# Performance work log

Hardware: AMD Instinct MI355X
Metric: run time of the kernel (lower is better)

## Reference

```python
import jax, jax.numpy as jnp
import numpy as np

E = float(np.e)  # torch.exp(torch.tensor(1.0))

def setup_inputs() -> dict:
    key = jax.random.key(0)
    k1, k2 = jax.random.split(key)
    b, t, d = 4, 4096, 256
    x = jax.random.normal(k1, (b, t, d), dtype=jnp.float32)
    padding_mask = jnp.zeros((b, 1, t), dtype=jnp.float32)  # additive mask: 0 valid, -inf-like for pad
    W_in = jax.random.normal(k2, (d, d), dtype=jnp.float32) * (1.0 / np.sqrt(d))
    b_in = jnp.zeros((d,), dtype=jnp.float32)
    return {"x": x, "padding_mask": padding_mask, "W_in": W_in, "b_in": b_in}

def reference(x, padding_mask, W_in, b_in):
    b, t, d = x.shape
    x = x @ W_in.T + b_in  # proj_in
    n = jnp.arange(1, t + 1, dtype=x.dtype)  # linspace(1,t,t)
    dist = jnp.abs(n[None, :] - n[:, None])  # [t,t] |i-j|
    tg = -dist[None, :, :] + padding_mask    # [b,t,t] via broadcast
    attn = jnp.exp(tg / E)                   # exponential distance decay, no softmax
    return jnp.matmul(attn, x)               # [b,t,d]
```

## Files before the change

kernel.cpp:

```cpp
#include <hip/hip_runtime.h>

#define TT 4096
#define DD 256
#define BT 64
#define HW 64
#define WIN (BT + 2*HW)
#define YP (DD + 8)
#define WP 40

typedef __attribute__((ext_vector_type(8))) short short8;
typedef __attribute__((ext_vector_type(4))) float f32x4;

__device__ __forceinline__ unsigned short f2bf(float f) {
    unsigned int u = __builtin_bit_cast(unsigned int, f);
    u += 0x7fffu + ((u >> 16) & 1u);
    return (unsigned short)(u >> 16);
}
__device__ __forceinline__ float bf2f(unsigned short h) {
    unsigned int u = ((unsigned int)h) << 16;
    return __builtin_bit_cast(float, u);
}

__global__ __launch_bounds__(512, 2)
void distattn_kernel(const float* __restrict__ x,
                     const float* __restrict__ mask,
                     const float* __restrict__ Win,
                     const float* __restrict__ bin,
                     float* __restrict__ out)
{
    __shared__ float yF[BT][DD + 1];
    __shared__ unsigned short yB[BT][YP];
    __shared__ unsigned short Wl[2][DD][WP];
    __shared__ float wv[WIN];
    __shared__ float rp[WIN];
    __shared__ float sp[8][BT];
    __shared__ float s_l[BT];

    const int tid  = threadIdx.x;
    const int b    = blockIdx.x >> 6;
    const int r0   = (blockIdx.x & 63) * BT;
    const int base = r0 - HW;

    const float INV_E = 0.36787944117144233f;
    const float R     = 0.69220062755534635f;

    if (tid < WIN) {
        rp[tid] = __expf(-(float)tid * INV_E);
        int j = base + tid;
        wv[tid] = (j >= 0 && j < TT) ? __expf(mask[b * TT + j] * INV_E) : 0.0f;
    }
    __syncthreads();

    if (tid < 256) {
        const int c = tid;
        const float* xb = x + (size_t)b * TT * DD + c;
        float f = 0.0f;
        #pragma unroll 8
        for (int t = 0; t < HW; ++t) {
            int jc = max(base + t, 0);
            f = fmaf(R, f, xb[(size_t)jc * DD] * wv[t]);
        }
        #pragma unroll 8
        for (int t = HW; t < HW + BT; ++t) {
            int j = base + t;
            f = fmaf(R, f, xb[(size_t)j * DD] * wv[t]);
            yF[t - HW][c] = f;
        }
    } else {
        const int c = tid - 256;
        const float* xb = x + (size_t)b * TT * DD + c;
        float bb = 0.0f;
        #pragma unroll 8
        for (int t = WIN - 1; t >= HW + BT; --t) {
            int jc = min(base + t, TT - 1);
            bb = fmaf(R, bb, xb[(size_t)jc * DD] * wv[t]);
        }
        #pragma unroll 8
        for (int t = HW + BT - 1; t >= HW; --t) {
            int j = base + t;
            float v = xb[(size_t)j * DD] * wv[t];
            bb = fmaf(R, bb, v);
            yB[t - HW][c] = f2bf(bb - v);
        }
    }

    {
        int row = tid & 63, q = tid >> 6;
        float s = 0.0f;
        #pragma unroll 8
        for (int tt = 0; tt < 24; ++tt) {
            int t = 24 * q + tt;
            int d = row + HW - t; d = (d < 0) ? -d : d;
            s = fmaf(rp[d], wv[t], s);
        }
        sp[q][row] = s;
    }

    auto stage = [&](int c, int bufsel) {
        #pragma unroll
        for (int it = 0; it < 4; ++it) {
            int e   = tid + (it << 9);
            int row = e >> 3;
            int kp  = e & 7;
            float4 w4 = *reinterpret_cast<const float4*>(&Win[row * DD + 32 * c + 4 * kp]);
            uint2 p;
            p.x = (unsigned)f2bf(w4.x) | ((unsigned)f2bf(w4.y) << 16);
            p.y = (unsigned)f2bf(w4.z) | ((unsigned)f2bf(w4.w) << 16);
            *reinterpret_cast<uint2*>(&Wl[bufsel][row][4 * kp]) = p;
        }
    };

    stage(0, 0);
    __syncthreads();

    #pragma unroll
    for (int e = 0; e < 32; ++e) {
        int idx = (e << 9) | tid;
        int i = idx >> 8, c = idx & 255;
        yB[i][c] = f2bf(yF[i][c] + bf2f(yB[i][c]));
    }
    if (tid < BT) {
        float s = 0.0f;
        #pragma unroll
        for (int q = 0; q < 8; ++q) s += sp[q][tid];
        s_l[tid] = s;
    }
    __syncthreads();

    const int w  = tid >> 6;
    const int lane = tid & 63;
    const int lr = lane & 15;
    const int lg = lane >> 4;
    const int wr = w >> 2;
    const int wc = w & 3;

    f32x4 acc[2][4];
    #pragma unroll
    for (int m = 0; m < 2; ++m)
        #pragma unroll
        for (int n = 0; n < 4; ++n) acc[m][n] = (f32x4){0.f, 0.f, 0.f, 0.f};

    for (int kk = 0; kk < 8; ++kk) {
        if (kk < 7) stage(kk + 1, (kk + 1) & 1);
        short8 afr[2], bfr[4];
        #pragma unroll
        for (int m = 0; m < 2; ++m)
            afr[m] = *reinterpret_cast<const short8*>(&yB[32 * wr + 16 * m + lr][kk * 32 + lg * 8]);
        #pragma unroll
        for (int n = 0; n < 4; ++n)
            bfr[n] = *reinterpret_cast<const short8*>(&Wl[kk & 1][64 * wc + 16 * n + lr][lg * 8]);
        #pragma unroll
        for (int m = 0; m < 2; ++m)
            #pragma unroll
            for (int n = 0; n < 4; ++n)
                acc[m][n] = __builtin_amdgcn_mfma_f32_16x16x32_bf16(afr[m], bfr[n], acc[m][n], 0, 0, 0);
        __syncthreads();
    }

    float bcol[4];
    #pragma unroll
    for (int n = 0; n < 4; ++n) bcol[n] = bin[64 * wc + 16 * n + lr];
    float* ob = out + ((size_t)b * TT + r0) * DD;
    #pragma unroll
    for (int m = 0; m < 2; ++m) {
        #pragma unroll
        for (int j = 0; j < 4; ++j) {
            int i = 32 * wr + 16 * m + lg * 4 + j;
            float si = s_l[i];
            #pragma unroll
            for (int n = 0; n < 4; ++n)
                ob[(size_t)i * DD + 64 * wc + 16 * n + lr] = acc[m][n][j] + si * bcol[n];
        }
    }
}

extern "C" void kernel_launch(void* const* d_in, const int* in_sizes, int n_in,
                              void* d_out, int out_size, void* d_ws, size_t ws_size,
                              hipStream_t stream) {
    const float* x    = (const float*)d_in[0];
    const float* mask = (const float*)d_in[1];
    const float* Win  = (const float*)d_in[2];
    const float* bin  = (const float*)d_in[3];
    float* out = (float*)d_out;

    const int nb = in_sizes[0] / (TT * DD);
    hipLaunchKernelGGL(distattn_kernel, dim3(nb * (TT / BT)), dim3(512), 0, stream,
                       x, mask, Win, bin, out);
}
```

Measured before the change: 25.25 us.

## Replace serial decay recurrences with banded MFMA matmul using split-bf16 inputs

The forward and backward exponential-decay scans over the 192-row window are replaced by a banded matrix product on MFMA. Decay weights come from a bf16 lookup table, and x is split into hi and lo bf16 parts to keep precision. The loads of x and W are double-buffered in registers and LDS with swizzled layouts, and blockIdx is remapped. This removes the long serial dependency chains, at the cost of extra MFMA work and bf16 rounding of the decay coefficients.

```diff
diff --git a/kernel.cpp b/kernel.cpp
--- a/kernel.cpp
+++ b/kernel.cpp
@@ -4,21 +4,23 @@
 #define DD 256
 #define BT 64
 #define HW 64
-#define WIN (BT + 2*HW)
-#define YP (DD + 8)
-#define WP 40
+#define WIN 192
 
 typedef __attribute__((ext_vector_type(8))) short short8;
 typedef __attribute__((ext_vector_type(4))) float f32x4;
-
-__device__ __forceinline__ unsigned short f2bf(float f) {
+typedef __attribute__((ext_vector_type(4))) unsigned int u32x4;
+
+__device__ __forceinline__ unsigned int f2bf(float f) {
     unsigned int u = __builtin_bit_cast(unsigned int, f);
     u += 0x7fffu + ((u >> 16) & 1u);
-    return (unsigned short)(u >> 16);
-}
-__device__ __forceinline__ float bf2f(unsigned short h) {
-    unsigned int u = ((unsigned int)h) << 16;
+    return u >> 16;
+}
+__device__ __forceinline__ float bf2f(unsigned int h) {
+    unsigned int u = h << 16;
     return __builtin_bit_cast(float, u);
+}
+__device__ __forceinline__ int qswz(int row, int q) {
+    return row * 64 + ((q ^ ((row >> 1) & 3)) << 4);
 }
 
 __global__ __launch_bounds__(512, 2)
@@ -28,66 +30,104 @@
                      const float* __restrict__ bin,
                      float* __restrict__ out)
 {
-    __shared__ float yF[BT][DD + 1];
-    __shared__ unsigned short yB[BT][YP];
-    __shared__ unsigned short Wl[2][DD][WP];
+    __shared__ __align__(16) unsigned short xT[2][256][32];
+    __shared__ __align__(16) unsigned short yB[64][256];
+    __shared__ __align__(16) unsigned short Wl[2][256][32];
     __shared__ float wv[WIN];
     __shared__ float rp[WIN];
+    __shared__ unsigned short rpb[WIN];
     __shared__ float sp[8][BT];
     __shared__ float s_l[BT];
 
     const int tid  = threadIdx.x;
-    const int b    = blockIdx.x >> 6;
-    const int r0   = (blockIdx.x & 63) * BT;
+    const int orig = blockIdx.x;
+    const int wg   = (orig & 7) * 32 + (orig >> 3);
+    const int b    = wg >> 6;
+    const int r0   = (wg & 63) * BT;
     const int base = r0 - HW;
 
+    const int w  = tid >> 6, lane = tid & 63;
+    const int lr = lane & 15, lg = lane >> 4;
+    const int wr = w >> 2,   wc = w & 3;
+
     const float INV_E = 0.36787944117144233f;
-    const float R     = 0.69220062755534635f;
 
     if (tid < WIN) {
-        rp[tid] = __expf(-(float)tid * INV_E);
+        float rv = __expf(-(float)tid * INV_E);
+        rp[tid]  = rv;
+        rpb[tid] = (unsigned short)f2bf(rv);
         int j = base + tid;
         wv[tid] = (j >= 0 && j < TT) ? __expf(mask[b * TT + j] * INV_E) : 0.0f;
     }
+
+    const int c    = tid >> 1;
+    const int half = tid & 1;
+    const float* xcol = x + (size_t)b * TT * DD + c;
+
+    auto xload = [&](int ch, float* xv) {
+        int t0 = ch * 16 + half * 8;
+        #pragma unroll
+        for (int s = 0; s < 8; ++s) {
+            int j = base + t0 + s;
+            j = min(max(j, 0), TT - 1);
+            xv[s] = xcol[(size_t)j * DD];
+        }
+    };
+    auto xstore = [&](int ch, const float* xv, int buf) {
+        int t0 = ch * 16 + half * 8;
+        unsigned int pk[8];
+        #pragma unroll
+        for (int s = 0; s < 8; ++s) {
+            float v = xv[s] * wv[t0 + s];
+            unsigned int hi = f2bf(v);
+            float lo = v - bf2f(hi);
+            pk[s] = (hi & 0xffffu) | (f2bf(lo) << 16);
+        }
+        char* bp = (char*)(&xT[buf][0][0]);
+        *(u32x4*)(bp + qswz(c, 2 * half))     = (u32x4){pk[0], pk[1], pk[2], pk[3]};
+        *(u32x4*)(bp + qswz(c, 2 * half + 1)) = (u32x4){pk[4], pk[5], pk[6], pk[7]};
+    };
+
+    f32x4 acc1[2][4];
+    #pragma unroll
+    for (int m = 0; m < 2; ++m)
+        #pragma unroll
+        for (int n = 0; n < 4; ++n) acc1[m][n] = (f32x4){0.f, 0.f, 0.f, 0.f};
+
+    auto p1mm = [&](int ch, int buf) {
+        short8 afr[2], bfr[4];
+        #pragma unroll
+        for (int m = 0; m < 2; ++m) {
+            int i = 32 * wr + 16 * m + lr;
+            unsigned short a[4];
+            #pragma unroll
+            for (int jj = 0; jj < 4; ++jj) {
+                int d = i + HW - (ch * 16 + 4 * lg + jj);
+                d = d < 0 ? -d : d;
+                a[jj] = rpb[d];
+            }
+            afr[m] = (short8){(short)a[0], (short)a[0], (short)a[1], (short)a[1],
+                              (short)a[2], (short)a[2], (short)a[3], (short)a[3]};
+        }
+        const char* bp = (const char*)(&xT[buf][0][0]);
+        #pragma unroll
+        for (int n = 0; n < 4; ++n)
+            bfr[n] = *(const short8*)(bp + qswz(64 * wc + 16 * n + lr, lg));
+        #pragma unroll
+        for (int m = 0; m < 2; ++m)
+            #pragma unroll
+            for (int n = 0; n < 4; ++n)
+                acc1[m][n] = __builtin_amdgcn_mfma_f32_16x16x32_bf16(afr[m], bfr[n], acc1[m][n], 0, 0, 0);
+    };
+
+    float rA[8], rB[8];
+    xload(0, rA);
     __syncthreads();
-
-    if (tid < 256) {
-        const int c = tid;
-        const float* xb = x + (size_t)b * TT * DD + c;
-        float f = 0.0f;
-        #pragma unroll 8
-        for (int t = 0; t < HW; ++t) {
-            int jc = max(base + t, 0);
-            f = fmaf(R, f, xb[(size_t)jc * DD] * wv[t]);
-        }
-        #pragma unroll 8
-        for (int t = HW; t < HW + BT; ++t) {
-            int j = base + t;
-            f = fmaf(R, f, xb[(size_t)j * DD] * wv[t]);
-            yF[t - HW][c] = f;
-        }
-    } else {
-        const int c = tid - 256;
-        const float* xb = x + (size_t)b * TT * DD + c;
-        float bb = 0.0f;
-        #pragma unroll 8
-        for (int t = WIN - 1; t >= HW + BT; --t) {
-            int jc = min(base + t, TT - 1);
-            bb = fmaf(R, bb, xb[(size_t)jc * DD] * wv[t]);
-        }
-        #pragma unroll 8
-        for (int t = HW + BT - 1; t >= HW; --t) {
-            int j = base + t;
-            float v = xb[(size_t)j * DD] * wv[t];
-            bb = fmaf(R, bb, v);
-            yB[t - HW][c] = f2bf(bb - v);
-        }
-    }
 
     {
         int row = tid & 63, q = tid >> 6;
         float s = 0.0f;
-        #pragma unroll 8
+        #pragma unroll
         for (int tt = 0; tt < 24; ++tt) {
             int t = 24 * q + tt;
             int d = row + HW - t; d = (d < 0) ? -d : d;
@@ -96,28 +136,64 @@
         sp[q][row] = s;
     }
 
-    auto stage = [&](int c, int bufsel) {
-        #pragma unroll
-        for (int it = 0; it < 4; ++it) {
-            int e   = tid + (it << 9);
-            int row = e >> 3;
-            int kp  = e & 7;
-            float4 w4 = *reinterpret_cast<const float4*>(&Win[row * DD + 32 * c + 4 * kp]);
-            uint2 p;
-            p.x = (unsigned)f2bf(w4.x) | ((unsigned)f2bf(w4.y) << 16);
-            p.y = (unsigned)f2bf(w4.z) | ((unsigned)f2bf(w4.w) << 16);
-            *reinterpret_cast<uint2*>(&Wl[bufsel][row][4 * kp]) = p;
-        }
-    };
-
-    stage(0, 0);
+    xstore(0, rA, 0);
+    xload(1, rA);
     __syncthreads();
 
-    #pragma unroll
-    for (int e = 0; e < 32; ++e) {
-        int idx = (e << 9) | tid;
-        int i = idx >> 8, c = idx & 255;
-        yB[i][c] = f2bf(yF[i][c] + bf2f(yB[i][c]));
+    #pragma unroll 1
+    for (int ch = 0; ch < 12; ch += 2) {
+        if (ch + 2 < 12) xload(ch + 2, rB);
+        p1mm(ch, 0);
+        xstore(ch + 1, rA, 1);
+        __syncthreads();
+
+        if (ch + 3 < 12) xload(ch + 3, rA);
+        p1mm(ch + 1, 1);
+        if (ch + 2 < 12) xstore(ch + 2, rB, 0);
+        __syncthreads();
+    }
+
+    auto wload = [&](int ch, float4* w4) {
+        #pragma unroll
+        for (int it = 0; it < 2; ++it) {
+            int U = tid + (it << 9);
+            int row = U >> 2, qu = U & 3;
+            const float* gp = Win + row * DD + 32 * ch + 8 * qu;
+            w4[2 * it]     = *(const float4*)(gp);
+            w4[2 * it + 1] = *(const float4*)(gp + 4);
+        }
+    };
+    auto wstore = [&](const float4* w4, int buf) {
+        char* bp = (char*)(&Wl[buf][0][0]);
+        #pragma unroll
+        for (int it = 0; it < 2; ++it) {
+            int U = tid + (it << 9);
+            int row = U >> 2, qu = U & 3;
+            unsigned int p0 = (f2bf(w4[2*it].x)   & 0xffffu) | (f2bf(w4[2*it].y)   << 16);
+            unsigned int p1 = (f2bf(w4[2*it].z)   & 0xffffu) | (f2bf(w4[2*it].w)   << 16);
+            unsigned int p2 = (f2bf(w4[2*it+1].x) & 0xffffu) | (f2bf(w4[2*it+1].y) << 16);
+            unsigned int p3 = (f2bf(w4[2*it+1].z) & 0xffffu) | (f2bf(w4[2*it+1].w) << 16);
+            *(u32x4*)(bp + qswz(row, qu)) = (u32x4){p0, p1, p2, p3};
+        }
+    };
+
+    float4 wA[4], wB[4];
+    wload(0, wA);
+
+    {
+        char* yp = (char*)(&yB[0][0]);
+        #pragma unroll
+        for (int m = 0; m < 2; ++m)
+            #pragma unroll
+            for (int j = 0; j < 4; ++j) {
+                int i = 32 * wr + 16 * m + 4 * lg + j;
+                #pragma unroll
+                for (int n = 0; n < 4; ++n) {
+                    int col = 64 * wc + 16 * n + lr;
+                    *(unsigned short*)(yp + i * 512 + (((col >> 3) ^ (i & 7)) << 4) + (col & 7) * 2)
+                        = (unsigned short)f2bf(acc1[m][n][j]);
+                }
+            }
     }
     if (tid < BT) {
         float s = 0.0f;
@@ -125,35 +201,45 @@
         for (int q = 0; q < 8; ++q) s += sp[q][tid];
         s_l[tid] = s;
     }
+    wstore(wA, 0);
+    wload(1, wA);
     __syncthreads();
 
-    const int w  = tid >> 6;
-    const int lane = tid & 63;
-    const int lr = lane & 15;
-    const int lg = lane >> 4;
-    const int wr = w >> 2;
-    const int wc = w & 3;
-
-    f32x4 acc[2][4];
+    f32x4 acc2[2][4];
     #pragma unroll
     for (int m = 0; m < 2; ++m)
         #pragma unroll
-        for (int n = 0; n < 4; ++n) acc[m][n] = (f32x4){0.f, 0.f, 0.f, 0.f};
-
-    for (int kk = 0; kk < 8; ++kk) {
-        if (kk < 7) stage(kk + 1, (kk + 1) & 1);
+        for (int n = 0; n < 4; ++n) acc2[m][n] = (f32x4){0.f, 0.f, 0.f, 0.f};
+
+    auto p2mm = [&](int kk, int buf) {
         short8 afr[2], bfr[4];
+        const char* yp = (const char*)(&yB[0][0]);
+        #pragma unroll
+        for (int m = 0; m < 2; ++m) {
+            int i = 32 * wr + 16 * m + lr;
+            afr[m] = *(const short8*)(yp + i * 512 + (((4 * kk + lg) ^ (i & 7)) << 4));
+        }
+        const char* bp = (const char*)(&Wl[buf][0][0]);
+        #pragma unroll
+        for (int n = 0; n < 4; ++n)
+            bfr[n] = *(const short8*)(bp + qswz(64 * wc + 16 * n + lr, lg));
         #pragma unroll
         for (int m = 0; m < 2; ++m)
-            afr[m] = *reinterpret_cast<const short8*>(&yB[32 * wr + 16 * m + lr][kk * 32 + lg * 8]);
-        #pragma unroll
-        for (int n = 0; n < 4; ++n)
-            bfr[n] = *reinterpret_cast<const short8*>(&Wl[kk & 1][64 * wc + 16 * n + lr][lg * 8]);
-        #pragma unroll
-        for (int m = 0; m < 2; ++m)
             #pragma unroll
             for (int n = 0; n < 4; ++n)
-                acc[m][n] = __builtin_amdgcn_mfma_f32_16x16x32_bf16(afr[m], bfr[n], acc[m][n], 0, 0, 0);
+                acc2[m][n] = __builtin_amdgcn_mfma_f32_16x16x32_bf16(afr[m], bfr[n], acc2[m][n], 0, 0, 0);
+    };
+
+    #pragma unroll 1
+    for (int kk = 0; kk < 8; kk += 2) {
+        if (kk + 2 < 8) wload(kk + 2, wB);
+        p2mm(kk, 0);
+        wstore(wA, 1);
+        __syncthreads();
+
+        if (kk + 3 < 8) wload(kk + 3, wA);
+        p2mm(kk + 1, 1);
+        if (kk + 2 < 8) wstore(wB, 0);
         __syncthreads();
     }
 
@@ -162,16 +248,15 @@
     for (int n = 0; n < 4; ++n) bcol[n] = bin[64 * wc + 16 * n + lr];
     float* ob = out + ((size_t)b * TT + r0) * DD;
     #pragma unroll
-    for (int m = 0; m < 2; ++m) {
+    for (int m = 0; m < 2; ++m)
         #pragma unroll
         for (int j = 0; j < 4; ++j) {
-            int i = 32 * wr + 16 * m + lg * 4 + j;
+            int i = 32 * wr + 16 * m + 4 * lg + j;
             float si = s_l[i];
             #pragma unroll
             for (int n = 0; n < 4; ++n)
-                ob[(size_t)i * DD + 64 * wc + 16 * n + lr] = acc[m][n][j] + si * bcol[n];
-        }
-    }
+                ob[(size_t)i * DD + 64 * wc + 16 * n + lr] = acc2[m][n][j] + si * bcol[n];
+        }
 }
 
 extern "C" void kernel_launch(void* const* d_in, const int* in_sizes, int n_in,
```

New measurement: 27.38 us. 8.5% more time.
